# Kernel tuning notes

Hardware: AMD Instinct MI355X
Metric: run time of the kernel (lower is better)

The kernel has to match this reference:

```python
import jax, jax.numpy as jnp
import numpy as np
import math

NUM_HEADS = 16
ROPE_BASE = 10000.0

def _rotate_half(t):
    d = t.shape[-1]
    x1, x2 = t[..., : d // 2], t[..., d // 2 :]
    return jnp.concatenate([-x2, x1], axis=-1)

def _rope_tables(seq_len, head_dim, dtype):
    inv_freq = 1.0 / (ROPE_BASE ** (jnp.arange(0, head_dim, 2, dtype=jnp.float32) / head_dim))
    t = jnp.arange(seq_len, dtype=jnp.float32)
    freqs = jnp.einsum('i,j->ij', t, inv_freq)          # [S, d/2]
    emb = jnp.concatenate([freqs, freqs], axis=-1)      # [S, d]
    return jnp.cos(emb).astype(dtype), jnp.sin(emb).astype(dtype)

def setup_inputs() -> dict:
    key = jax.random.key(0)
    ks = jax.random.split(key, 6)
    B, S, HID = 4, 2048, 1024
    x = jax.random.normal(ks[0], (B, S, HID), dtype=jnp.float32)
    w_scale = 0.02
    Wq = jax.random.normal(ks[1], (HID, HID), dtype=jnp.float32) * w_scale
    Wk = jax.random.normal(ks[2], (HID, HID), dtype=jnp.float32) * w_scale
    Wv = jax.random.normal(ks[3], (HID, HID), dtype=jnp.float32) * w_scale
    Wo = jax.random.normal(ks[4], (HID, HID), dtype=jnp.float32) * w_scale
    # ragged valid lengths in [S//2, S] so each sequence is non-trivial
    seq_lens = jax.random.randint(ks[5], (B,), S // 2, S + 1, dtype=jnp.int32)
    return {"x": x, "Wq": Wq, "Wk": Wk, "Wv": Wv, "Wo": Wo, "seq_lens": seq_lens}

def reference(x, Wq, Wk, Wv, Wo, seq_lens):
    B, S, HID = x.shape
    H = NUM_HEADS
    d = HID // H
    scale = 1.0 / math.sqrt(d)

    # qkv projections (nn.Linear, no bias)
    q = (x @ Wq).reshape(B, S, H, d)
    k = (x @ Wk).reshape(B, S, H, d)
    v = (x @ Wv).reshape(B, S, H, d)

    # fused RoPE, positions start at 0 for every sequence (prefill, beg=0)
    cos, sin = _rope_tables(S, d, x.dtype)              # [S, d]
    cos = cos[None, :, None, :]
    sin = sin[None, :, None, :]
    q = q * cos + _rotate_half(q) * sin
    k = k * cos + _rotate_half(k) * sin

    # causal SDPA over ragged batch via padding masks
    scores = jnp.einsum('bqhd,bkhd->bhqk', q, k) * scale  # [B,H,S,S]
    pos = jnp.arange(S)
    causal = pos[:, None] >= pos[None, :]                 # [S,S]
    valid_k = pos[None, :] < seq_lens[:, None]            # [B,S]
    mask = causal[None, None, :, :] & valid_k[:, None, None, :]
    neg = jnp.asarray(-1e9, dtype=scores.dtype)
    attn = jax.nn.softmax(jnp.where(mask, scores, neg), axis=-1)
    out = jnp.einsum('bhqk,bkhd->bqhd', attn, v).reshape(B, S, HID)

    out = out @ Wo
    # zero out padded query positions (they do not exist in CatTensor)
    valid_q = (pos[None, :] < seq_lens[:, None])[..., None]
    return jnp.where(valid_q, out, jnp.zeros((), dtype=out.dtype))
```

## Files before the change

### kernel.cpp

```cpp
#include <hip/hip_runtime.h>
#include <hip/hip_bf16.h>

typedef __attribute__((ext_vector_type(8))) short short8;
typedef __attribute__((ext_vector_type(4))) float f32x4;

constexpr int Bc   = 4;
constexpr int Sc   = 2048;
constexpr int HIDc = 1024;
constexpr int Hc   = 16;
constexpr size_t FB = (size_t)Bc * Sc * HIDc;

__device__ __forceinline__ int get_L(const int* seq, int b)
{
    return (seq[1] == 0) ? seq[2 * b] : seq[b];
}

__device__ __forceinline__ short f2bf(float v)
{
    __hip_bfloat16 h = __float2bfloat16(v);
    return *reinterpret_cast<short*>(&h);
}
__device__ __forceinline__ float bf2f(short s)
{
    __hip_bfloat16 h = *reinterpret_cast<__hip_bfloat16*>(&s);
    return __bfloat162float(h);
}

__global__ __launch_bounds__(256) void split_pass(const float* __restrict__ in,
                                                  short* __restrict__ hi,
                                                  short* __restrict__ lo)
{
    const size_t i8 = ((size_t)blockIdx.x * 256 + threadIdx.x) * 8;
    const float4 u0 = *(const float4*)(in + i8);
    const float4 u1 = *(const float4*)(in + i8 + 4);
    const float v[8] = {u0.x, u0.y, u0.z, u0.w, u1.x, u1.y, u1.z, u1.w};
    short8 h, l;
#pragma unroll
    for (int j = 0; j < 8; j++) {
        const short hb = f2bf(v[j]);
        h[j] = hb;
        l[j] = f2bf(v[j] - bf2f(hb));
    }
    *(short8*)(hi + i8) = h;
    *(short8*)(lo + i8) = l;
}

__global__ __launch_bounds__(256) void rope_split(const float* __restrict__ p,
                                                  short* __restrict__ hi,
                                                  short* __restrict__ lo)
{
    const int idx = blockIdx.x * 256 + threadIdx.x;
    const int jc = idx & 3;
    const int h  = (idx >> 2) & 15;
    const int s  = (idx >> 6) & 2047;
    const int b  = idx >> 17;
    const int j0 = jc * 8;
    const size_t base = ((size_t)(b * Sc + s)) * HIDc + h * 64 + j0;

    const float4 a0 = *(const float4*)(p + base);
    const float4 a1 = *(const float4*)(p + base + 4);
    const float4 b0 = *(const float4*)(p + base + 32);
    const float4 b1 = *(const float4*)(p + base + 36);
    const float x1[8] = {a0.x, a0.y, a0.z, a0.w, a1.x, a1.y, a1.z, a1.w};
    const float x2[8] = {b0.x, b0.y, b0.z, b0.w, b1.x, b1.y, b1.z, b1.w};

    short8 h1, h2, l1, l2;
#pragma unroll
    for (int jj = 0; jj < 8; jj++) {
        const int j = j0 + jj;
        const float ang = (float)s * powf(10000.0f, -(float)j * (1.0f / 32.0f));
        const float cv = cosf(ang);
        const float sv = sinf(ang);
        const float y1 = x1[jj] * cv - x2[jj] * sv;
        const float y2 = x2[jj] * cv + x1[jj] * sv;
        const short hb1 = f2bf(y1), hb2 = f2bf(y2);
        h1[jj] = hb1; l1[jj] = f2bf(y1 - bf2f(hb1));
        h2[jj] = hb2; l2[jj] = f2bf(y2 - bf2f(hb2));
    }
    *(short8*)(hi + base)      = h1;
    *(short8*)(hi + base + 32) = h2;
    *(short8*)(lo + base)      = l1;
    *(short8*)(lo + base + 32) = l2;
}

__global__ __launch_bounds__(256) void vsplit_t(const float* __restrict__ V,
                                                short* __restrict__ th,
                                                short* __restrict__ tl)
{
    __shared__ float T[64][65];
    const int s0 = blockIdx.x * 64;
    const int h  = blockIdx.y & 15;
    const int b  = blockIdx.y >> 4;
    const int t  = threadIdx.x;
    const int r  = t >> 2;
    const int c  = (t & 3) * 16;
#pragma unroll
    for (int j = 0; j < 4; j++) {
        const float4 u = *(const float4*)(V + ((size_t)(b * Sc + s0 + r)) * HIDc + h * 64 + c + j * 4);
        T[r][c + j * 4 + 0] = u.x; T[r][c + j * 4 + 1] = u.y;
        T[r][c + j * 4 + 2] = u.z; T[r][c + j * 4 + 3] = u.w;
    }
    __syncthreads();
    short8 h0, h1, l0, l1;
#pragma unroll
    for (int j = 0; j < 8; j++) {
        const float v = T[c + j][r];
        const short hb = f2bf(v);
        h0[j] = hb; l0[j] = f2bf(v - bf2f(hb));
    }
#pragma unroll
    for (int j = 0; j < 8; j++) {
        const float v = T[c + 8 + j][r];
        const short hb = f2bf(v);
        h1[j] = hb; l1[j] = f2bf(v - bf2f(hb));
    }
    const size_t dst = ((size_t)(b * Hc + h) * 64 + r) * Sc + s0 + c;
    *(short8*)(th + dst)     = h0;
    *(short8*)(th + dst + 8) = h1;
    *(short8*)(tl + dst)     = l0;
    *(short8*)(tl + dst + 8) = l1;
}

__global__ __launch_bounds__(256) void wsplit_t(const float* __restrict__ W,
                                                short* __restrict__ th,
                                                short* __restrict__ tl)
{
    __shared__ float T[64][65];
    const int t  = threadIdx.x;
    const int n0 = blockIdx.x * 64;
    const int k0 = blockIdx.y * 64;
    const int r  = t >> 2;
    const int c  = (t & 3) * 16;
#pragma unroll
    for (int j = 0; j < 4; j++) {
        const float4 u = *(const float4*)(W + (size_t)(k0 + r) * HIDc + n0 + c + j * 4);
        T[r][c + j * 4 + 0] = u.x; T[r][c + j * 4 + 1] = u.y;
        T[r][c + j * 4 + 2] = u.z; T[r][c + j * 4 + 3] = u.w;
    }
    __syncthreads();
    short8 h0, h1, l0, l1;
#pragma unroll
    for (int j = 0; j < 8; j++) {
        const float v = T[c + j][r];
        const short hb = f2bf(v);
        h0[j] = hb; l0[j] = f2bf(v - bf2f(hb));
    }
#pragma unroll
    for (int j = 0; j < 8; j++) {
        const float v = T[c + 8 + j][r];
        const short hb = f2bf(v);
        h1[j] = hb; l1[j] = f2bf(v - bf2f(hb));
    }
    const size_t dst = (size_t)(n0 + r) * HIDc + k0 + c;
    *(short8*)(th + dst)     = h0;
    *(short8*)(th + dst + 8) = h1;
    *(short8*)(tl + dst)     = l0;
    *(short8*)(tl + dst + 8) = l1;
}

__global__ __launch_bounds__(256, 2) void gemm_x3(
    const short* __restrict__ Ah, const short* __restrict__ Al,
    const short* __restrict__ Bh, const short* __restrict__ Bl,
    float* __restrict__ C, const int* __restrict__ seq)
{
    __shared__ alignas(16) short AhS[128 * 64];
    __shared__ alignas(16) short AlS[128 * 64];
    __shared__ alignas(16) short BhS[128 * 64];
    __shared__ alignas(16) short BlS[128 * 64];

    const int t    = threadIdx.x;
    const int lane = t & 63;
    const int wid  = t >> 6;
    const int wr   = (wid >> 1) * 64;
    const int wc   = (wid & 1) * 64;
    const int lr   = lane & 15;
    const int lg   = lane >> 4;
    const int m0   = blockIdx.y * 128;
    const int n0   = blockIdx.x * 128;

    f32x4 acc[4][4];
#pragma unroll
    for (int mi = 0; mi < 4; mi++)
#pragma unroll
        for (int ni = 0; ni < 4; ni++) acc[mi][ni] = (f32x4)(0.f);

    for (int k0 = 0; k0 < HIDc; k0 += 64) {
        __syncthreads();
#pragma unroll
        for (int i = 0; i < 4; i++) {
            const int o  = i * 4096 + t * 16;
            const int r  = o >> 7;
            const int sc = (o & 127) ^ ((r & 7) << 4);
            const int k  = sc >> 1;
            const size_t ga = (size_t)(m0 + r) * HIDc + k0 + k;
            const size_t gb = (size_t)(n0 + r) * HIDc + k0 + k;
            __builtin_amdgcn_global_load_lds(
                (const __attribute__((address_space(1))) void*)(Ah + ga),
                (__attribute__((address_space(3))) void*)((char*)AhS + o), 16, 0, 0);
            __builtin_amdgcn_global_load_lds(
                (const __attribute__((address_space(1))) void*)(Al + ga),
                (__attribute__((address_space(3))) void*)((char*)AlS + o), 16, 0, 0);
            __builtin_amdgcn_global_load_lds(
                (const __attribute__((address_space(1))) void*)(Bh + gb),
                (__attribute__((address_space(3))) void*)((char*)BhS + o), 16, 0, 0);
            __builtin_amdgcn_global_load_lds(
                (const __attribute__((address_space(1))) void*)(Bl + gb),
                (__attribute__((address_space(3))) void*)((char*)BlS + o), 16, 0, 0);
        }
        __syncthreads();

        short8 a_h[4][2], a_l[4][2];
#pragma unroll
        for (int mi = 0; mi < 4; mi++) {
            const int r = wr + mi * 16 + lr;
#pragma unroll
            for (int kk = 0; kk < 2; kk++) {
                const int cb  = kk * 64 + lg * 16;
                const int off = r * 128 + (cb ^ ((r & 7) << 4));
                a_h[mi][kk] = *(const short8*)((const char*)AhS + off);
                a_l[mi][kk] = *(const short8*)((const char*)AlS + off);
            }
        }
#pragma unroll
        for (int ni = 0; ni < 4; ni++) {
            const int rn = wc + ni * 16 + lr;
            short8 b_h[2], b_l[2];
#pragma unroll
            for (int kk = 0; kk < 2; kk++) {
                const int cb  = kk * 64 + lg * 16;
                const int off = rn * 128 + (cb ^ ((rn & 7) << 4));
                b_h[kk] = *(const short8*)((const char*)BhS + off);
                b_l[kk] = *(const short8*)((const char*)BlS + off);
            }
#pragma unroll
            for (int mi = 0; mi < 4; mi++) {
#pragma unroll
                for (int kk = 0; kk < 2; kk++) {
                    acc[mi][ni] = __builtin_amdgcn_mfma_f32_16x16x32_bf16(
                        a_h[mi][kk], b_h[kk], acc[mi][ni], 0, 0, 0);
                    acc[mi][ni] = __builtin_amdgcn_mfma_f32_16x16x32_bf16(
                        a_h[mi][kk], b_l[kk], acc[mi][ni], 0, 0, 0);
                    acc[mi][ni] = __builtin_amdgcn_mfma_f32_16x16x32_bf16(
                        a_l[mi][kk], b_h[kk], acc[mi][ni], 0, 0, 0);
                }
            }
        }
    }

#pragma unroll
    for (int mi = 0; mi < 4; mi++) {
#pragma unroll
        for (int rr = 0; rr < 4; rr++) {
            const int row = m0 + wr + mi * 16 + lg * 4 + rr;
            bool zero = false;
            if (seq != nullptr) zero = ((row & 2047) >= get_L(seq, row >> 11));
#pragma unroll
            for (int ni = 0; ni < 4; ni++) {
                const float v = zero ? 0.f : acc[mi][ni][rr];
                C[(size_t)row * HIDc + n0 + wc + ni * 16 + lr] = v;
            }
        }
    }
}

__global__ __launch_bounds__(256, 3) void attn_mfma(
    const short* __restrict__ Qh, const short* __restrict__ Ql,
    const short* __restrict__ Kh, const short* __restrict__ Kl,
    const short* __restrict__ Vth, const short* __restrict__ Vtl,
    short* __restrict__ Oh, short* __restrict__ Ol,
    const int* __restrict__ seq)
{
    __shared__ alignas(16) short KhS[64 * 64];
    __shared__ alignas(16) short KlS[64 * 64];
    __shared__ alignas(16) short VhS[64 * 64];
    __shared__ alignas(16) short VlS[64 * 64];
    __shared__ alignas(16) short PhS[4][16 * 64];
    __shared__ alignas(16) short PlS[4][16 * 64];

    const int blk  = blockIdx.x;
    const int bh   = blk & 63;
    const int qt   = 31 - (blk >> 6);
    const int h    = bh & 15;
    const int b    = bh >> 4;
    const int q0   = qt * 64;
    const int L    = get_L(seq, b);
    const int t    = threadIdx.x;
    const int w    = t >> 6;
    const int lane = t & 63;
    const int lr   = lane & 15;
    const int lg   = lane >> 4;

    if (q0 >= L) {
        const int r = t >> 2;
        const int c = (t & 3) * 16;
        const size_t base = ((size_t)(b * Sc + q0 + r)) * HIDc + h * 64 + c;
        const short8 z = {0, 0, 0, 0, 0, 0, 0, 0};
        *(short8*)(Oh + base)     = z;
        *(short8*)(Oh + base + 8) = z;
        *(short8*)(Ol + base)     = z;
        *(short8*)(Ol + base + 8) = z;
        return;
    }

    short8 qa_h[2], qa_l[2];
    {
        const size_t qrow = ((size_t)(b * Sc + q0 + w * 16 + lr)) * HIDc + h * 64;
        qa_h[0] = *(const short8*)(Qh + qrow + lg * 8);
        qa_h[1] = *(const short8*)(Qh + qrow + 32 + lg * 8);
        qa_l[0] = *(const short8*)(Ql + qrow + lg * 8);
        qa_l[1] = *(const short8*)(Ql + qrow + 32 + lg * 8);
    }

    f32x4 oacc[4];
#pragma unroll
    for (int t2 = 0; t2 < 4; t2++) oacc[t2] = (f32x4)(0.f);
    float m_i[4], l_i[4];
#pragma unroll
    for (int r = 0; r < 4; r++) { m_i[r] = -1.0e30f; l_i[r] = 0.f; }

    const int kend = min(q0 + 64, L);
    for (int kb = 0; kb < kend; kb += 64) {
        __syncthreads();
#pragma unroll
        for (int i = 0; i < 2; i++) {
            const int o  = i * 4096 + t * 16;
            const int r  = o >> 7;
            const int sc = (o & 127) ^ ((r & 7) << 4);
            const int k  = sc >> 1;
            const size_t gk = ((size_t)(b * Sc + kb + r)) * HIDc + h * 64 + k;
            const size_t gv = ((size_t)(b * Hc + h) * 64 + r) * Sc + kb + k;
            __builtin_amdgcn_global_load_lds(
                (const __attribute__((address_space(1))) void*)(Kh + gk),
                (__attribute__((address_space(3))) void*)((char*)KhS + o), 16, 0, 0);
            __builtin_amdgcn_global_load_lds(
                (const __attribute__((address_space(1))) void*)(Kl + gk),
                (__attribute__((address_space(3))) void*)((char*)KlS + o), 16, 0, 0);
            __builtin_amdgcn_global_load_lds(
                (const __attribute__((address_space(1))) void*)(Vth + gv),
                (__attribute__((address_space(3))) void*)((char*)VhS + o), 16, 0, 0);
            __builtin_amdgcn_global_load_lds(
                (const __attribute__((address_space(1))) void*)(Vtl + gv),
                (__attribute__((address_space(3))) void*)((char*)VlS + o), 16, 0, 0);
        }
        __syncthreads();

        f32x4 s4[4];
#pragma unroll
        for (int tt = 0; tt < 4; tt++) s4[tt] = (f32x4)(0.f);
        __builtin_amdgcn_s_setprio(1);
#pragma unroll
        for (int tt = 0; tt < 4; tt++) {
            const int rn = tt * 16 + lr;
#pragma unroll
            for (int kk = 0; kk < 2; kk++) {
                const int off = rn * 128 + ((kk * 64 + lg * 16) ^ ((rn & 7) << 4));
                const short8 kb_h = *(const short8*)((const char*)KhS + off);
                const short8 kb_l = *(const short8*)((const char*)KlS + off);
                s4[tt] = __builtin_amdgcn_mfma_f32_16x16x32_bf16(qa_h[kk], kb_h, s4[tt], 0, 0, 0);
                s4[tt] = __builtin_amdgcn_mfma_f32_16x16x32_bf16(qa_h[kk], kb_l, s4[tt], 0, 0, 0);
                s4[tt] = __builtin_amdgcn_mfma_f32_16x16x32_bf16(qa_l[kk], kb_h, s4[tt], 0, 0, 0);
            }
        }
        __builtin_amdgcn_s_setprio(0);

#pragma unroll
        for (int r = 0; r < 4; r++) {
            const int qpos = q0 + w * 16 + lg * 4 + r;
            float sv[4];
#pragma unroll
            for (int tt = 0; tt < 4; tt++) {
                const int kpos = kb + tt * 16 + lr;
                const bool valid = (kpos <= qpos) && (kpos < L);
                sv[tt] = valid ? s4[tt][r] * 0.125f : -1.0e9f;
            }
            float tm = fmaxf(fmaxf(sv[0], sv[1]), fmaxf(sv[2], sv[3]));
#pragma unroll
            for (int off = 1; off < 16; off <<= 1)
                tm = fmaxf(tm, __shfl_xor(tm, off));
            const float mnew  = fmaxf(m_i[r], tm);
            const float alpha = __expf(m_i[r] - mnew);

            float psum = 0.f;
#pragma unroll
            for (int tt = 0; tt < 4; tt++) {
                sv[tt] = __expf(sv[tt] - mnew);
                psum += sv[tt];
            }
#pragma unroll
            for (int off = 1; off < 16; off <<= 1)
                psum += __shfl_xor(psum, off);

            l_i[r] = alpha * l_i[r] + psum;
            m_i[r] = mnew;
#pragma unroll
            for (int t2 = 0; t2 < 4; t2++) oacc[t2][r] *= alpha;

            const int q = lg * 4 + r;
#pragma unroll
            for (int tt = 0; tt < 4; tt++) {
                const int off = q * 128 + (((tt * 16 + lr) * 2) ^ ((q & 7) << 4));
                const float pv = sv[tt];
                const short ph = f2bf(pv);
                *(short*)((char*)&PhS[w][0] + off) = ph;
                *(short*)((char*)&PlS[w][0] + off) = f2bf(pv - bf2f(ph));
            }
        }

        __builtin_amdgcn_sched_barrier(0);

        short8 pa_h[2], pa_l[2];
#pragma unroll
        for (int kk = 0; kk < 2; kk++) {
            const int poff = lr * 128 + ((kk * 64 + lg * 16) ^ ((lr & 7) << 4));
            pa_h[kk] = *(const short8*)((const char*)&PhS[w][0] + poff);
            pa_l[kk] = *(const short8*)((const char*)&PlS[w][0] + poff);
        }
        __builtin_amdgcn_s_setprio(1);
#pragma unroll
        for (int t2 = 0; t2 < 4; t2++) {
            const int rv = t2 * 16 + lr;
#pragma unroll
            for (int kk = 0; kk < 2; kk++) {
                const int voff = rv * 128 + ((kk * 64 + lg * 16) ^ ((rv & 7) << 4));
                const short8 vb_h = *(const short8*)((const char*)VhS + voff);
                const short8 vb_l = *(const short8*)((const char*)VlS + voff);
                oacc[t2] = __builtin_amdgcn_mfma_f32_16x16x32_bf16(pa_h[kk], vb_h, oacc[t2], 0, 0, 0);
                oacc[t2] = __builtin_amdgcn_mfma_f32_16x16x32_bf16(pa_h[kk], vb_l, oacc[t2], 0, 0, 0);
                oacc[t2] = __builtin_amdgcn_mfma_f32_16x16x32_bf16(pa_l[kk], vb_h, oacc[t2], 0, 0, 0);
            }
        }
        __builtin_amdgcn_s_setprio(0);
    }

#pragma unroll
    for (int r = 0; r < 4; r++) {
        const float inv = 1.0f / l_i[r];
        const int row = q0 + w * 16 + lg * 4 + r;
        const size_t base = ((size_t)(b * Sc + row)) * HIDc + h * 64;
#pragma unroll
        for (int t2 = 0; t2 < 4; t2++) {
            const float v = oacc[t2][r] * inv;
            const short hb = f2bf(v);
            Oh[base + t2 * 16 + lr] = hb;
            Ol[base + t2 * 16 + lr] = f2bf(v - bf2f(hb));
        }
    }
}

__global__ __launch_bounds__(256) void gemm64(
    const float* __restrict__ A, const float* __restrict__ W,
    float* __restrict__ C, const int K, const int N,
    const int* __restrict__ seq)
{
    __shared__ float As[32][68];
    __shared__ float Bs[32][68];

    const int t  = threadIdx.x;
    const int m0 = blockIdx.y * 64;
    const int n0 = blockIdx.x * 64;
    const int ty = t >> 4, tx = t & 15;
    const int ar = t >> 2;
    const int ac = (t & 3) * 8;
    const int wr = t >> 3;
    const int wc = (t & 7) * 8;

    float acc[4][4];
#pragma unroll
    for (int i = 0; i < 4; i++)
#pragma unroll
        for (int j = 0; j < 4; j++) acc[i][j] = 0.f;

    for (int k0 = 0; k0 < K; k0 += 32) {
        __syncthreads();
        {
            const float* p = A + (size_t)(m0 + ar) * K + k0 + ac;
            const float4 u0 = *(const float4*)p;
            const float4 u1 = *(const float4*)(p + 4);
            As[ac + 0][ar] = u0.x; As[ac + 1][ar] = u0.y;
            As[ac + 2][ar] = u0.z; As[ac + 3][ar] = u0.w;
            As[ac + 4][ar] = u1.x; As[ac + 5][ar] = u1.y;
            As[ac + 6][ar] = u1.z; As[ac + 7][ar] = u1.w;
        }
        {
            const float* p = W + (size_t)(k0 + wr) * N + n0 + wc;
            const float4 u0 = *(const float4*)p;
            const float4 u1 = *(const float4*)(p + 4);
            *(float4*)&Bs[wr][wc]     = u0;
            *(float4*)&Bs[wr][wc + 4] = u1;
        }
        __syncthreads();

#pragma unroll 8
        for (int kk = 0; kk < 32; kk++) {
            const float4 a4 = *(const float4*)&As[kk][ty * 4];
            const float4 b4 = *(const float4*)&Bs[kk][tx * 4];
            const float av[4] = {a4.x, a4.y, a4.z, a4.w};
            const float bv[4] = {b4.x, b4.y, b4.z, b4.w};
#pragma unroll
            for (int i = 0; i < 4; i++)
#pragma unroll
                for (int j = 0; j < 4; j++)
                    acc[i][j] = fmaf(av[i], bv[j], acc[i][j]);
        }
    }

#pragma unroll
    for (int i = 0; i < 4; i++) {
        const int row = m0 + ty * 4 + i;
        bool zero = false;
        if (seq != nullptr) zero = ((row & 2047) >= get_L(seq, row >> 11));
#pragma unroll
        for (int j = 0; j < 4; j++) {
            const float v = zero ? 0.f : acc[i][j];
            C[(size_t)row * N + n0 + tx * 4 + j] = v;
        }
    }
}

__global__ __launch_bounds__(256) void rope_pair(float* __restrict__ p)
{
    const int idx = blockIdx.x * 256 + threadIdx.x;
    const int j = idx & 31;
    const int h = (idx >> 5) & 15;
    const int s = (idx >> 9) & 2047;
    const int b = idx >> 20;
    const size_t base = ((size_t)(b * Sc + s)) * HIDc + h * 64 + j;

    const float x1 = p[base];
    const float x2 = p[base + 32];
    const float ang = (float)s * powf(10000.0f, -(float)j * (1.0f / 32.0f));
    const float cv = cosf(ang);
    const float sv = sinf(ang);
    p[base]      = x1 * cv - x2 * sv;
    p[base + 32] = x2 * cv + x1 * sv;
}

__device__ __forceinline__ int swz(int r, int chunk)
{
    return (((chunk ^ (r >> 2)) & 15) << 2);
}

__global__ __launch_bounds__(256) void attn64(
    const float* Q, const float* __restrict__ K,
    const float* __restrict__ V, float* O,
    const int* __restrict__ seq)
{
    __shared__ float Qs[64][64];
    __shared__ float Ks[64][64];
    __shared__ float Vs[64][64];

    const int blk = blockIdx.x;
    const int bh  = blk & 63;
    const int qt  = 31 - (blk >> 6);
    const int h   = bh & 15;
    const int b   = bh >> 4;
    const int q0  = qt * 64;
    const int L   = get_L(seq, b);
    const int t   = threadIdx.x;
    const int qg  = t >> 4;
    const int kg  = t & 15;

    if (q0 >= L) {
#pragma unroll
        for (int i = 0; i < 4; i++) {
            const size_t row = (size_t)(b * Sc + q0 + qg * 4 + i);
#pragma unroll
            for (int c = 0; c < 4; c++)
                O[row * HIDc + h * 64 + kg * 4 + c] = 0.f;
        }
        return;
    }

    {
        const int r = t >> 2;
        const int c = (t & 3) * 16;
        const float* src = Q + ((size_t)(b * Sc + q0 + r)) * HIDc + h * 64 + c;
#pragma unroll
        for (int jj = 0; jj < 4; jj++)
            *(float4*)&Qs[r][swz(r, (c >> 2) + jj)] = *(const float4*)(src + 4 * jj);
    }

    float m_i[4], l_i[4], acc[4][4];
#pragma unroll
    for (int i = 0; i < 4; i++) {
        m_i[i] = -1.0e30f; l_i[i] = 0.f;
#pragma unroll
        for (int c = 0; c < 4; c++) acc[i][c] = 0.f;
    }

    const int kend = min(q0 + 64, L);
    for (int kb = 0; kb < kend; kb += 64) {
        __syncthreads();
        {
            const int r = t >> 2;
            const int c = (t & 3) * 16;
            const size_t off = ((size_t)(b * Sc + kb + r)) * HIDc + h * 64 + c;
#pragma unroll
            for (int jj = 0; jj < 4; jj++)
                *(float4*)&Ks[r][swz(r, (c >> 2) + jj)] = *(const float4*)(K + off + 4 * jj);
#pragma unroll
            for (int jj = 0; jj < 4; jj++)
                *(float4*)&Vs[r][swz(r, (c >> 2) + jj)] = *(const float4*)(V + off + 4 * jj);
        }
        __syncthreads();

        float s[4][4];
#pragma unroll
        for (int i = 0; i < 4; i++)
#pragma unroll
            for (int c = 0; c < 4; c++) s[i][c] = 0.f;

#pragma unroll 4
        for (int dc = 0; dc < 64; dc += 4) {
            float4 q4[4], k4[4];
#pragma unroll
            for (int i = 0; i < 4; i++)
                q4[i] = *(const float4*)&Qs[qg * 4 + i][swz(qg * 4 + i, dc >> 2)];
#pragma unroll
            for (int c = 0; c < 4; c++)
                k4[c] = *(const float4*)&Ks[kg * 4 + c][swz(kg * 4 + c, dc >> 2)];
#pragma unroll
            for (int i = 0; i < 4; i++)
#pragma unroll
                for (int c = 0; c < 4; c++) {
                    s[i][c] = fmaf(q4[i].x, k4[c].x, s[i][c]);
                    s[i][c] = fmaf(q4[i].y, k4[c].y, s[i][c]);
                    s[i][c] = fmaf(q4[i].z, k4[c].z, s[i][c]);
                    s[i][c] = fmaf(q4[i].w, k4[c].w, s[i][c]);
                }
        }

#pragma unroll
        for (int i = 0; i < 4; i++) {
            const int qpos = q0 + qg * 4 + i;
#pragma unroll
            for (int c = 0; c < 4; c++) {
                const int kpos = kb + kg * 4 + c;
                const bool valid = (kpos <= qpos) && (kpos < L);
                s[i][c] = valid ? s[i][c] * 0.125f : -1.0e9f;
            }
        }

#pragma unroll
        for (int i = 0; i < 4; i++) {
            float tm = fmaxf(fmaxf(s[i][0], s[i][1]), fmaxf(s[i][2], s[i][3]));
#pragma unroll
            for (int off = 1; off < 16; off <<= 1)
                tm = fmaxf(tm, __shfl_xor(tm, off));
            const float mnew  = fmaxf(m_i[i], tm);
            const float alpha = __expf(m_i[i] - mnew);

            float psum = 0.f;
#pragma unroll
            for (int c = 0; c < 4; c++) {
                s[i][c] = __expf(s[i][c] - mnew);
                psum += s[i][c];
            }
#pragma unroll
            for (int off = 1; off < 16; off <<= 1)
                psum += __shfl_xor(psum, off);

            l_i[i] = alpha * l_i[i] + psum;
            m_i[i] = mnew;
#pragma unroll
            for (int c = 0; c < 4; c++) acc[i][c] *= alpha;
        }

        __syncthreads();
#pragma unroll
        for (int i = 0; i < 4; i++)
#pragma unroll
            for (int c = 0; c < 4; c++) {
                const int pr = kg * 4 + c;
                Ks[pr][swz(pr, qg) + i] = s[i][c];
            }
        __syncthreads();

#pragma unroll 4
        for (int ki = 0; ki < 64; ki++) {
            const float4 p4 = *(const float4*)&Ks[ki][swz(ki, qg)];
            const float4 v4 = *(const float4*)&Vs[ki][swz(ki, kg)];
            const float pv[4] = {p4.x, p4.y, p4.z, p4.w};
            const float vv[4] = {v4.x, v4.y, v4.z, v4.w};
#pragma unroll
            for (int i = 0; i < 4; i++)
#pragma unroll
                for (int c = 0; c < 4; c++)
                    acc[i][c] = fmaf(pv[i], vv[c], acc[i][c]);
        }
    }

#pragma unroll
    for (int i = 0; i < 4; i++) {
        const float inv = 1.0f / l_i[i];
        const size_t row = (size_t)(b * Sc + q0 + qg * 4 + i);
#pragma unroll
        for (int c = 0; c < 4; c++)
            O[row * HIDc + h * 64 + kg * 4 + c] = acc[i][c] * inv;
    }
}

extern "C" void kernel_launch(void* const* d_in, const int* in_sizes, int n_in,
                              void* d_out, int out_size, void* d_ws, size_t ws_size,
                              hipStream_t stream)
{
    const float* x   = (const float*)d_in[0];
    const float* Wq  = (const float*)d_in[1];
    const float* Wk  = (const float*)d_in[2];
    const float* Wv  = (const float*)d_in[3];
    const float* Wo  = (const float*)d_in[4];
    const int*   seq = (const int*)d_in[5];

    const size_t WN     = (size_t)HIDc * HIDc;
    const size_t needX3 = 3 * FB * sizeof(float) + 2 * WN * sizeof(short);

    if (ws_size >= needX3) {
        float* Qf = (float*)d_ws;
        float* Kf = Qf + FB;
        float* Vf = Kf + FB;
        short* ws_s = (short*)d_ws;
        short* wh = ws_s + 6 * FB;
        short* wl = wh + WN;

        short* xh = (short*)d_out;
        short* xl = xh + FB;

        const dim3 wg(16, 16);
        const dim3 gg(HIDc / 128, Bc * Sc / 128);
        const int  sb = (int)(FB / (8 * 256));
        const int  rsb = (int)(FB / (16 * 256));

        split_pass<<<sb, 256, 0, stream>>>(x, xh, xl);

        wsplit_t<<<wg, 256, 0, stream>>>(Wq, wh, wl);
        gemm_x3<<<gg, 256, 0, stream>>>(xh, xl, wh, wl, Qf, nullptr);
        wsplit_t<<<wg, 256, 0, stream>>>(Wk, wh, wl);
        gemm_x3<<<gg, 256, 0, stream>>>(xh, xl, wh, wl, Kf, nullptr);
        wsplit_t<<<wg, 256, 0, stream>>>(Wv, wh, wl);
        gemm_x3<<<gg, 256, 0, stream>>>(xh, xl, wh, wl, Vf, nullptr);

        short* Qh2 = (short*)d_out;
        short* Ql2 = Qh2 + FB;
        rope_split<<<rsb, 256, 0, stream>>>(Qf, Qh2, Ql2);
        short* Kh2 = ws_s;
        short* Kl2 = Kh2 + FB;
        rope_split<<<rsb, 256, 0, stream>>>(Kf, Kh2, Kl2);
        short* Vth = ws_s + 2 * FB;
        short* Vtl = Vth + FB;
        vsplit_t<<<dim3(32, 64), 256, 0, stream>>>(Vf, Vth, Vtl);

        short* Oh2 = ws_s + 4 * FB;
        short* Ol2 = Oh2 + FB;
        attn_mfma<<<Bc * Hc * (Sc / 64), 256, 0, stream>>>(
            Qh2, Ql2, Kh2, Kl2, Vth, Vtl, Oh2, Ol2, seq);

        wsplit_t<<<wg, 256, 0, stream>>>(Wo, wh, wl);
        gemm_x3<<<gg, 256, 0, stream>>>(Oh2, Ol2, wh, wl, (float*)d_out, seq);
    } else if (ws_size >= 3 * FB * sizeof(float)) {
        float* Q = (float*)d_ws;
        float* K = Q + FB;
        float* V = K + FB;

        const dim3 gg(HIDc / 64, Bc * Sc / 64);
        gemm64<<<gg, 256, 0, stream>>>(x, Wq, Q, HIDc, HIDc, nullptr);
        gemm64<<<gg, 256, 0, stream>>>(x, Wk, K, HIDc, HIDc, nullptr);
        gemm64<<<gg, 256, 0, stream>>>(x, Wv, V, HIDc, HIDc, nullptr);

        const int rb = Bc * Sc * Hc * 32 / 256;
        rope_pair<<<rb, 256, 0, stream>>>(Q);
        rope_pair<<<rb, 256, 0, stream>>>(K);

        attn64<<<Bc * Hc * (Sc / 64), 256, 0, stream>>>(Q, K, V, Q, seq);

        gemm64<<<gg, 256, 0, stream>>>(Q, Wo, (float*)d_out, HIDc, HIDc, seq);
    } else {
        hipMemsetAsync(d_out, 0, (size_t)out_size * sizeof(float), stream);
    }
}
```

Measured before the change: 448.5 us.

## Batch weight splits and QKV GEMMs; swap attention MFMA operands for lane-local softmax

Weight hi/lo splitting for all four matrices now runs in one launch, and the three QKV projections run as a single batched GEMM launch over a z-dimension. Both replace several small serial launches and give larger grids. Attention now computes S^T by swapping the MFMA operands, so each lane owns one query row. Row max and sum then need only two cross-lane shuffles instead of a 4-step reduction per row, and P is written to LDS as packed 8-byte stores. The new path needs more workspace (eight weight buffers) and falls back to the old path if that space is not available.

```diff
diff --git a/kernel.cpp b/kernel.cpp
--- a/kernel.cpp
+++ b/kernel.cpp
@@ -9,6 +9,7 @@
 constexpr int HIDc = 1024;
 constexpr int Hc   = 16;
 constexpr size_t FB = (size_t)Bc * Sc * HIDc;
+constexpr size_t WN = (size_t)HIDc * HIDc;
 
 __device__ __forceinline__ int get_L(const int* seq, int b)
 {
@@ -24,6 +25,10 @@
 {
     __hip_bfloat16 h = *reinterpret_cast<__hip_bfloat16*>(&s);
     return __bfloat162float(h);
+}
+__device__ __forceinline__ unsigned pack2(short a, short b)
+{
+    return (unsigned)(unsigned short)a | ((unsigned)(unsigned short)b << 16);
 }
 
 __global__ __launch_bounds__(256) void split_pass(const float* __restrict__ in,
@@ -121,11 +126,11 @@
     *(short8*)(tl + dst + 8) = l1;
 }
 
-__global__ __launch_bounds__(256) void wsplit_t(const float* __restrict__ W,
-                                                short* __restrict__ th,
-                                                short* __restrict__ tl)
-{
-    __shared__ float T[64][65];
+__device__ __forceinline__ void wsplit_body(const float* __restrict__ W,
+                                            short* __restrict__ th,
+                                            short* __restrict__ tl,
+                                            float (*T)[65])
+{
     const int t  = threadIdx.x;
     const int n0 = blockIdx.x * 64;
     const int k0 = blockIdx.y * 64;
@@ -158,16 +163,32 @@
     *(short8*)(tl + dst + 8) = l1;
 }
 
-__global__ __launch_bounds__(256, 2) void gemm_x3(
+__global__ __launch_bounds__(256) void wsplit_t(const float* __restrict__ W,
+                                                short* __restrict__ th,
+                                                short* __restrict__ tl)
+{
+    __shared__ float T[64][65];
+    wsplit_body(W, th, tl, T);
+}
+
+__global__ __launch_bounds__(256) void wsplit4_t(
+    const float* __restrict__ W0, const float* __restrict__ W1,
+    const float* __restrict__ W2, const float* __restrict__ W3,
+    short* __restrict__ out)
+{
+    __shared__ float T[64][65];
+    const int z = blockIdx.z;
+    const float* W = (z == 0) ? W0 : (z == 1) ? W1 : (z == 2) ? W2 : W3;
+    short* th = out + (size_t)z * 2 * WN;
+    wsplit_body(W, th, th + WN, T);
+}
+
+__device__ __forceinline__ void gemm_x3_body(
     const short* __restrict__ Ah, const short* __restrict__ Al,
     const short* __restrict__ Bh, const short* __restrict__ Bl,
-    float* __restrict__ C, const int* __restrict__ seq)
-{
-    __shared__ alignas(16) short AhS[128 * 64];
-    __shared__ alignas(16) short AlS[128 * 64];
-    __shared__ alignas(16) short BhS[128 * 64];
-    __shared__ alignas(16) short BlS[128 * 64];
-
+    float* __restrict__ C, const int* __restrict__ seq,
+    short* AhS, short* AlS, short* BhS, short* BlS)
+{
     const int t    = threadIdx.x;
     const int lane = t & 63;
     const int wid  = t >> 6;
@@ -196,16 +217,16 @@
             const size_t gb = (size_t)(n0 + r) * HIDc + k0 + k;
             __builtin_amdgcn_global_load_lds(
                 (const __attribute__((address_space(1))) void*)(Ah + ga),
-                (__attribute__((address_space(3))) void*)((char*)AhS + o), 16, 0, 0);
+                (__attribute__((address_space(3))) void*)(AhS + (o >> 1)), 16, 0, 0);
             __builtin_amdgcn_global_load_lds(
                 (const __attribute__((address_space(1))) void*)(Al + ga),
-                (__attribute__((address_space(3))) void*)((char*)AlS + o), 16, 0, 0);
+                (__attribute__((address_space(3))) void*)(AlS + (o >> 1)), 16, 0, 0);
             __builtin_amdgcn_global_load_lds(
                 (const __attribute__((address_space(1))) void*)(Bh + gb),
-                (__attribute__((address_space(3))) void*)((char*)BhS + o), 16, 0, 0);
+                (__attribute__((address_space(3))) void*)(BhS + (o >> 1)), 16, 0, 0);
             __builtin_amdgcn_global_load_lds(
                 (const __attribute__((address_space(1))) void*)(Bl + gb),
-                (__attribute__((address_space(3))) void*)((char*)BlS + o), 16, 0, 0);
+                (__attribute__((address_space(3))) void*)(BlS + (o >> 1)), 16, 0, 0);
         }
         __syncthreads();
 
@@ -263,7 +284,32 @@
     }
 }
 
-__global__ __launch_bounds__(256, 3) void attn_mfma(
+__global__ __launch_bounds__(256, 2) void gemm_x3(
+    const short* __restrict__ Ah, const short* __restrict__ Al,
+    const short* __restrict__ Bh, const short* __restrict__ Bl,
+    float* __restrict__ C, const int* __restrict__ seq)
+{
+    __shared__ alignas(16) short AhS[128 * 64];
+    __shared__ alignas(16) short AlS[128 * 64];
+    __shared__ alignas(16) short BhS[128 * 64];
+    __shared__ alignas(16) short BlS[128 * 64];
+    gemm_x3_body(Ah, Al, Bh, Bl, C, seq, AhS, AlS, BhS, BlS);
+}
+
+__global__ __launch_bounds__(256, 2) void gemm_x3_qkv(
+    const short* __restrict__ Ah, const short* __restrict__ Al,
+    const short* __restrict__ Wbase, float* __restrict__ Cbase)
+{
+    __shared__ alignas(16) short AhS[128 * 64];
+    __shared__ alignas(16) short AlS[128 * 64];
+    __shared__ alignas(16) short BhS[128 * 64];
+    __shared__ alignas(16) short BlS[128 * 64];
+    const short* Bh = Wbase + (size_t)blockIdx.z * 2 * WN;
+    gemm_x3_body(Ah, Al, Bh, Bh + WN, Cbase + (size_t)blockIdx.z * FB,
+                 nullptr, AhS, AlS, BhS, BlS);
+}
+
+__global__ __launch_bounds__(256, 3) void attn_mfma_sw(
     const short* __restrict__ Qh, const short* __restrict__ Ql,
     const short* __restrict__ Kh, const short* __restrict__ Kl,
     const short* __restrict__ Vth, const short* __restrict__ Vtl,
@@ -302,21 +348,21 @@
         return;
     }
 
-    short8 qa_h[2], qa_l[2];
+    short8 qb_h[2], qb_l[2];
     {
         const size_t qrow = ((size_t)(b * Sc + q0 + w * 16 + lr)) * HIDc + h * 64;
-        qa_h[0] = *(const short8*)(Qh + qrow + lg * 8);
-        qa_h[1] = *(const short8*)(Qh + qrow + 32 + lg * 8);
-        qa_l[0] = *(const short8*)(Ql + qrow + lg * 8);
-        qa_l[1] = *(const short8*)(Ql + qrow + 32 + lg * 8);
+        qb_h[0] = *(const short8*)(Qh + qrow + lg * 8);
+        qb_h[1] = *(const short8*)(Qh + qrow + 32 + lg * 8);
+        qb_l[0] = *(const short8*)(Ql + qrow + lg * 8);
+        qb_l[1] = *(const short8*)(Ql + qrow + 32 + lg * 8);
     }
 
     f32x4 oacc[4];
 #pragma unroll
     for (int t2 = 0; t2 < 4; t2++) oacc[t2] = (f32x4)(0.f);
-    float m_i[4], l_i[4];
-#pragma unroll
-    for (int r = 0; r < 4; r++) { m_i[r] = -1.0e30f; l_i[r] = 0.f; }
+    float m_s = -1.0e30f, l_s = 0.f;
+
+    const int qpos = q0 + w * 16 + lr;
 
     const int kend = min(q0 + 64, L);
     for (int kb = 0; kb < kend; kb += 64) {
@@ -354,56 +400,62 @@
 #pragma unroll
             for (int kk = 0; kk < 2; kk++) {
                 const int off = rn * 128 + ((kk * 64 + lg * 16) ^ ((rn & 7) << 4));
-                const short8 kb_h = *(const short8*)((const char*)KhS + off);
-                const short8 kb_l = *(const short8*)((const char*)KlS + off);
-                s4[tt] = __builtin_amdgcn_mfma_f32_16x16x32_bf16(qa_h[kk], kb_h, s4[tt], 0, 0, 0);
-                s4[tt] = __builtin_amdgcn_mfma_f32_16x16x32_bf16(qa_h[kk], kb_l, s4[tt], 0, 0, 0);
-                s4[tt] = __builtin_amdgcn_mfma_f32_16x16x32_bf16(qa_l[kk], kb_h, s4[tt], 0, 0, 0);
+                const short8 ka_h = *(const short8*)((const char*)KhS + off);
+                const short8 ka_l = *(const short8*)((const char*)KlS + off);
+                s4[tt] = __builtin_amdgcn_mfma_f32_16x16x32_bf16(ka_h, qb_h[kk], s4[tt], 0, 0, 0);
+                s4[tt] = __builtin_amdgcn_mfma_f32_16x16x32_bf16(ka_h, qb_l[kk], s4[tt], 0, 0, 0);
+                s4[tt] = __builtin_amdgcn_mfma_f32_16x16x32_bf16(ka_l, qb_h[kk], s4[tt], 0, 0, 0);
             }
         }
         __builtin_amdgcn_s_setprio(0);
 
+        float tmax = -1.0e30f;
+#pragma unroll
+        for (int tt = 0; tt < 4; tt++)
+#pragma unroll
+            for (int r = 0; r < 4; r++) {
+                const int kpos = kb + tt * 16 + lg * 4 + r;
+                const bool valid = (kpos <= qpos) && (kpos < L);
+                const float v = valid ? s4[tt][r] * 0.125f : -1.0e9f;
+                s4[tt][r] = v;
+                tmax = fmaxf(tmax, v);
+            }
+        tmax = fmaxf(tmax, __shfl_xor(tmax, 16));
+        tmax = fmaxf(tmax, __shfl_xor(tmax, 32));
+        const float mnew  = fmaxf(m_s, tmax);
+        const float alpha = __expf(m_s - mnew);
+        float psum = 0.f;
+#pragma unroll
+        for (int tt = 0; tt < 4; tt++)
+#pragma unroll
+            for (int r = 0; r < 4; r++) {
+                const float e = __expf(s4[tt][r] - mnew);
+                s4[tt][r] = e;
+                psum += e;
+            }
+        psum += __shfl_xor(psum, 16);
+        psum += __shfl_xor(psum, 32);
+        l_s = alpha * l_s + psum;
+        m_s = mnew;
+
 #pragma unroll
         for (int r = 0; r < 4; r++) {
-            const int qpos = q0 + w * 16 + lg * 4 + r;
-            float sv[4];
-#pragma unroll
-            for (int tt = 0; tt < 4; tt++) {
-                const int kpos = kb + tt * 16 + lr;
-                const bool valid = (kpos <= qpos) && (kpos < L);
-                sv[tt] = valid ? s4[tt][r] * 0.125f : -1.0e9f;
-            }
-            float tm = fmaxf(fmaxf(sv[0], sv[1]), fmaxf(sv[2], sv[3]));
-#pragma unroll
-            for (int off = 1; off < 16; off <<= 1)
-                tm = fmaxf(tm, __shfl_xor(tm, off));
-            const float mnew  = fmaxf(m_i[r], tm);
-            const float alpha = __expf(m_i[r] - mnew);
-
-            float psum = 0.f;
-#pragma unroll
-            for (int tt = 0; tt < 4; tt++) {
-                sv[tt] = __expf(sv[tt] - mnew);
-                psum += sv[tt];
-            }
-#pragma unroll
-            for (int off = 1; off < 16; off <<= 1)
-                psum += __shfl_xor(psum, off);
-
-            l_i[r] = alpha * l_i[r] + psum;
-            m_i[r] = mnew;
-#pragma unroll
-            for (int t2 = 0; t2 < 4; t2++) oacc[t2][r] *= alpha;
-
-            const int q = lg * 4 + r;
-#pragma unroll
-            for (int tt = 0; tt < 4; tt++) {
-                const int off = q * 128 + (((tt * 16 + lr) * 2) ^ ((q & 7) << 4));
-                const float pv = sv[tt];
-                const short ph = f2bf(pv);
-                *(short*)((char*)&PhS[w][0] + off) = ph;
-                *(short*)((char*)&PlS[w][0] + off) = f2bf(pv - bf2f(ph));
-            }
+            const float ar = __shfl(alpha, lg * 4 + r);
+#pragma unroll
+            for (int t2 = 0; t2 < 4; t2++) oacc[t2][r] *= ar;
+        }
+
+#pragma unroll
+        for (int tt = 0; tt < 4; tt++) {
+            const short h0 = f2bf(s4[tt][0]); const short l0 = f2bf(s4[tt][0] - bf2f(h0));
+            const short h1 = f2bf(s4[tt][1]); const short l1 = f2bf(s4[tt][1] - bf2f(h1));
+            const short h2 = f2bf(s4[tt][2]); const short l2 = f2bf(s4[tt][2] - bf2f(h2));
+            const short h3 = f2bf(s4[tt][3]); const short l3 = f2bf(s4[tt][3] - bf2f(h3));
+            const int off = lr * 128 + ((tt * 32 + lg * 8) ^ ((lr & 7) << 4));
+            uint2 uh; uh.x = pack2(h0, h1); uh.y = pack2(h2, h3);
+            uint2 ul; ul.x = pack2(l0, l1); ul.y = pack2(l2, l3);
+            *(uint2*)((char*)&PhS[w][0] + off) = uh;
+            *(uint2*)((char*)&PlS[w][0] + off) = ul;
         }
 
         __builtin_amdgcn_sched_barrier(0);
@@ -434,8 +486,9 @@
 
 #pragma unroll
     for (int r = 0; r < 4; r++) {
-        const float inv = 1.0f / l_i[r];
-        const int row = q0 + w * 16 + lg * 4 + r;
+        const float lrow = __shfl(l_s, lg * 4 + r);
+        const float inv  = 1.0f / lrow;
+        const int   row  = q0 + w * 16 + lg * 4 + r;
         const size_t base = ((size_t)(b * Sc + row)) * HIDc + h * 64;
 #pragma unroll
         for (int t2 = 0; t2 < 4; t2++) {
@@ -711,33 +764,26 @@
     const float* Wo  = (const float*)d_in[4];
     const int*   seq = (const int*)d_in[5];
 
-    const size_t WN     = (size_t)HIDc * HIDc;
     const size_t needX3 = 3 * FB * sizeof(float) + 2 * WN * sizeof(short);
-
-    if (ws_size >= needX3) {
+    const size_t needX4 = 3 * FB * sizeof(float) + 8 * WN * sizeof(short);
+
+    const dim3 gg(HIDc / 128, Bc * Sc / 128);
+    const int  sb  = (int)(FB / (8 * 256));
+    const int  rsb = (int)(FB / (16 * 256));
+
+    if (ws_size >= needX4) {
         float* Qf = (float*)d_ws;
         float* Kf = Qf + FB;
         float* Vf = Kf + FB;
         short* ws_s = (short*)d_ws;
-        short* wh = ws_s + 6 * FB;
-        short* wl = wh + WN;
+        short* W4 = ws_s + 6 * FB;
 
         short* xh = (short*)d_out;
         short* xl = xh + FB;
 
-        const dim3 wg(16, 16);
-        const dim3 gg(HIDc / 128, Bc * Sc / 128);
-        const int  sb = (int)(FB / (8 * 256));
-        const int  rsb = (int)(FB / (16 * 256));
-
         split_pass<<<sb, 256, 0, stream>>>(x, xh, xl);
-
-        wsplit_t<<<wg, 256, 0, stream>>>(Wq, wh, wl);
-        gemm_x3<<<gg, 256, 0, stream>>>(xh, xl, wh, wl, Qf, nullptr);
-        wsplit_t<<<wg, 256, 0, stream>>>(Wk, wh, wl);
-        gemm_x3<<<gg, 256, 0, stream>>>(xh, xl, wh, wl, Kf, nullptr);
-        wsplit_t<<<wg, 256, 0, stream>>>(Wv, wh, wl);
-        gemm_x3<<<gg, 256, 0, stream>>>(xh, xl, wh, wl, Vf, nullptr);
+        wsplit4_t<<<dim3(16, 16, 4), 256, 0, stream>>>(Wq, Wk, Wv, Wo, W4);
+        gemm_x3_qkv<<<dim3(8, 64, 3), 256, 0, stream>>>(xh, xl, W4, Qf);
 
         short* Qh2 = (short*)d_out;
         short* Ql2 = Qh2 + FB;
@@ -751,7 +797,46 @@
 
         short* Oh2 = ws_s + 4 * FB;
         short* Ol2 = Oh2 + FB;
-        attn_mfma<<<Bc * Hc * (Sc / 64), 256, 0, stream>>>(
+        attn_mfma_sw<<<Bc * Hc * (Sc / 64), 256, 0, stream>>>(
+            Qh2, Ql2, Kh2, Kl2, Vth, Vtl, Oh2, Ol2, seq);
+
+        gemm_x3<<<gg, 256, 0, stream>>>(Oh2, Ol2, W4 + 6 * WN, W4 + 7 * WN,
+                                        (float*)d_out, seq);
+    } else if (ws_size >= needX3) {
+        float* Qf = (float*)d_ws;
+        float* Kf = Qf + FB;
+        float* Vf = Kf + FB;
+        short* ws_s = (short*)d_ws;
+        short* wh = ws_s + 6 * FB;
+        short* wl = wh + WN;
+
+        short* xh = (short*)d_out;
+        short* xl = xh + FB;
+
+        const dim3 wg(16, 16);
+
+        split_pass<<<sb, 256, 0, stream>>>(x, xh, xl);
+
+        wsplit_t<<<wg, 256, 0, stream>>>(Wq, wh, wl);
+        gemm_x3<<<gg, 256, 0, stream>>>(xh, xl, wh, wl, Qf, nullptr);
+        wsplit_t<<<wg, 256, 0, stream>>>(Wk, wh, wl);
+        gemm_x3<<<gg, 256, 0, stream>>>(xh, xl, wh, wl, Kf, nullptr);
+        wsplit_t<<<wg, 256, 0, stream>>>(Wv, wh, wl);
+        gemm_x3<<<gg, 256, 0, stream>>>(xh, xl, wh, wl, Vf, nullptr);
+
+        short* Qh2 = (short*)d_out;
+        short* Ql2 = Qh2 + FB;
+        rope_split<<<rsb, 256, 0, stream>>>(Qf, Qh2, Ql2);
+        short* Kh2 = ws_s;
+        short* Kl2 = Kh2 + FB;
+        rope_split<<<rsb, 256, 0, stream>>>(Kf, Kh2, Kl2);
+        short* Vth = ws_s + 2 * FB;
+        short* Vtl = Vth + FB;
+        vsplit_t<<<dim3(32, 64), 256, 0, stream>>>(Vf, Vth, Vtl);
+
+        short* Oh2 = ws_s + 4 * FB;
+        short* Ol2 = Oh2 + FB;
+        attn_mfma_sw<<<Bc * Hc * (Sc / 64), 256, 0, stream>>>(
             Qh2, Ql2, Kh2, Kl2, Vth, Vtl, Oh2, Ol2, seq);
 
         wsplit_t<<<wg, 256, 0, stream>>>(Wo, wh, wl);
@@ -761,10 +846,10 @@
         float* K = Q + FB;
         float* V = K + FB;
 
-        const dim3 gg(HIDc / 64, Bc * Sc / 64);
-        gemm64<<<gg, 256, 0, stream>>>(x, Wq, Q, HIDc, HIDc, nullptr);
-        gemm64<<<gg, 256, 0, stream>>>(x, Wk, K, HIDc, HIDc, nullptr);
-        gemm64<<<gg, 256, 0, stream>>>(x, Wv, V, HIDc, HIDc, nullptr);
+        const dim3 g64(HIDc / 64, Bc * Sc / 64);
+        gemm64<<<g64, 256, 0, stream>>>(x, Wq, Q, HIDc, HIDc, nullptr);
+        gemm64<<<g64, 256, 0, stream>>>(x, Wk, K, HIDc, HIDc, nullptr);
+        gemm64<<<g64, 256, 0, stream>>>(x, Wv, V, HIDc, HIDc, nullptr);
 
         const int rb = Bc * Sc * Hc * 32 / 256;
         rope_pair<<<rb, 256, 0, stream>>>(Q);
@@ -772,7 +857,7 @@
 
         attn64<<<Bc * Hc * (Sc / 64), 256, 0, stream>>>(Q, K, V, Q, seq);
 
-        gemm64<<<gg, 256, 0, stream>>>(Q, Wo, (float*)d_out, HIDc, HIDc, seq);
+        gemm64<<<g64, 256, 0, stream>>>(Q, Wo, (float*)d_out, HIDc, HIDc, seq);
     } else {
         hipMemsetAsync(d_out, 0, (size_t)out_size * sizeof(float), stream);
     }
```

Result: faster. 417.1 us (-7.0%).
